# Optimization experiments

Measured on AMD Instinct MI355X. Metric: run time of the kernel, lower is better.

The kernel has to match this reference:

```python
import jax, jax.numpy as jnp
import numpy as np

MEAN, STD = 0.1307, 0.3081  # standard MNIST Normalization layer
FC = [784, 2048, 2048, 2048, 2048, 10]


def _forward_boxes(W, b, low, high):
    # swap bounds where weights are negative (interval arithmetic)
    Wn = jnp.where(W < 0, W, 0.0)
    Wp = jnp.where(W >= 0, W, 0.0)
    low_out = high @ Wn.T + low @ Wp.T + b
    high_out = low @ Wn.T + high @ Wp.T + b
    return low_out, high_out


def _abstract_relu(x, low, high):
    # vectorized DeepPoly relaxation (original loops per neuron)
    crossing = (low < 0) & (high > 0)
    denom = jnp.where(crossing, high - low, 1.0)  # safe denom
    ub_slope = jnp.where(crossing, high / denom, 0.0)
    ub_int = jnp.where(crossing, -(low * high) / denom, 0.0)
    lam = jnp.where(low * low > high * high, 0.0, 1.0)  # minimum-area lambda
    keep = jnp.where(high <= 0.0, 0.0, 1.0)  # identity diag unless dead neuron
    w_high = jnp.where(crossing, ub_slope, keep)
    w_low = jnp.where(crossing, lam, keep)
    b_high = ub_int
    x_out = jnp.maximum(x, 0.0)
    return x_out, w_low * low, w_high * high + b_high, (w_low, w_high, b_high)


def _back_sub_relu(M, w_high, w_low, b_high, is_high):
    # vectorized version of the original double python loop; w_* are the
    # relu diagonals ([in]), M is the accumulated backsub matrix [out,in]
    mask = (w_high != 0.0).astype(M.dtype)
    if is_high:
        out = jnp.where(M > 0, M * w_high, M * w_low) * mask
        bias = (jnp.maximum(M, 0.0) * mask) @ b_high
    else:
        out = jnp.where(M > 0, M * w_low, M * w_high) * mask
        bias = (jnp.minimum(M, 0.0) * mask) @ b_high
    return out, bias


def _back_sub(records, low0, high0, out_size):
    dt = low0.dtype
    Wl = jnp.eye(out_size, dtype=dt)
    Wh = jnp.eye(out_size, dtype=dt)
    bl = jnp.zeros(out_size, dtype=dt)
    bh = jnp.zeros(out_size, dtype=dt)
    for kind, data in reversed(records):
        if kind == 'linear':
            W, b = data
            bh = bh + Wh @ b
            bl = bl + Wl @ b
            Wh = Wh @ W
            Wl = Wl @ W
        else:  # relu
            wl, wh, bhr = data
            Wh, dbh = _back_sub_relu(Wh, wh, wl, bhr, True)
            Wl, dbl = _back_sub_relu(Wl, wh, wl, bhr, False)
            bh = bh + dbh
            bl = bl + dbl
    low_out, _ = _forward_boxes(Wl, bl, low0, high0)
    _, high_out = _forward_boxes(Wh, bh, low0, high0)
    return low_out, high_out


def _forward(x, low, high, params):
    norm = lambda t: ((t - MEAN) / STD).reshape(-1)
    x, low, high = norm(x), norm(low), norm(high)
    low0, high0 = low, high
    records = []
    n = len(params)
    for i, (W, b) in enumerate(params):
        x = W @ x + b
        records.append(('linear', (W, b)))
        # box bounds from forward_boxes are immediately replaced by backsub
        low, high = _back_sub(records, low0, high0, W.shape[0])
        if i + 1 < n:
            x, low, high, rdata = _abstract_relu(x, low, high)
            records.append(('relu', rdata))
    return x, low, high


def setup_inputs() -> dict:
    key = jax.random.key(0)
    ks = jax.random.split(key, 11)
    x = jax.random.normal(ks[0], (1, 1, 28, 28), dtype=jnp.float32)
    eps = 0.05
    inp = {"x": x, "low": x - eps, "high": x + eps}
    for i in range(5):
        fi, fo = FC[i], FC[i + 1]
        inp[f"W{i+1}"] = jax.random.normal(ks[1 + 2 * i], (fo, fi), dtype=jnp.float32) * float(1.0 / np.sqrt(fi))
        inp[f"b{i+1}"] = jax.random.normal(ks[2 + 2 * i], (fo,), dtype=jnp.float32) * 0.01
    return inp


def reference(x, low, high, W1, b1, W2, b2, W3, b3, W4, b4, W5, b5):
    params = [(W1, b1), (W2, b2), (W3, b3), (W4, b4), (W5, b5)]
    return _forward(x, low, high, params)
```

## Files before the change

### kernel.cpp

```cpp
#include <hip/hip_runtime.h>
#include <hip/hip_bf16.h>


#define MEAN_C 0.1307f
#define STD_C  0.3081f

#define OFF_X0     0u
#define OFF_X1     2048u
#define OFF_L0     4096u
#define OFF_H0     5120u
#define OFF_WL     6144u
#define OFF_WH     14336u
#define OFF_BHR    22528u
#define OFF_BOX    30720u
#define OFF_BIAS   34816u
#define OFF_B20    38912u
#define OFF_PPA    38944u
#define OFF_PPB    366624u
#define OFF_PPC    694304u
#define OFF_PPD    1021984u
#define OFF_WTH    1349664u
#define OFF_WTL    3446816u
#define OFF_AH0    5543968u
#define OFF_AL0    9738272u
#define OFF_AH1    13932576u
#define OFF_AL1    18126880u

typedef _Float16 half8 __attribute__((ext_vector_type(8)));
typedef float floatx4 __attribute__((ext_vector_type(4)));

__device__ __forceinline__ void gl2lds16(const void* g, void* l) {
    __builtin_amdgcn_global_load_lds(
        (const __attribute__((address_space(1))) unsigned int*)g,
        (__attribute__((address_space(3))) unsigned int*)l, 16, 0, 0);
}

__device__ __forceinline__ float blockReduce256(float v) {
    #pragma unroll
    for (int o = 32; o > 0; o >>= 1) v += __shfl_down(v, o, 64);
    __shared__ float sred[4];
    int w = threadIdx.x >> 6;
    if ((threadIdx.x & 63) == 0) sred[w] = v;
    __syncthreads();
    float r = 0.f;
    if (threadIdx.x == 0) r = sred[0] + sred[1] + sred[2] + sred[3];
    return r;
}

__device__ __forceinline__ float2 blockReduce256x2(float a, float b) {
    #pragma unroll
    for (int o = 32; o > 0; o >>= 1) {
        a += __shfl_down(a, o, 64);
        b += __shfl_down(b, o, 64);
    }
    __shared__ float sa[4], sb[4];
    int w = threadIdx.x >> 6;
    if ((threadIdx.x & 63) == 0) { sa[w] = a; sb[w] = b; }
    __syncthreads();
    float2 r = {0.f, 0.f};
    if (threadIdx.x == 0) {
        r.x = sa[0] + sa[1] + sa[2] + sa[3];
        r.y = sb[0] + sb[1] + sb[2] + sb[3];
    }
    return r;
}

__global__ void k_norm(const float* __restrict__ x, const float* __restrict__ lo,
                       const float* __restrict__ hi, float* __restrict__ ws) {
    int i = blockIdx.x * blockDim.x + threadIdx.x;
    if (i < 784) {
        ws[OFF_X0 + i] = (x[i]  - MEAN_C) / STD_C;
        ws[OFF_L0 + i] = (lo[i] - MEAN_C) / STD_C;
        ws[OFF_H0 + i] = (hi[i] - MEAN_C) / STD_C;
    } else if (i < 896) {
        ws[OFF_L0 + i] = 0.f;
        ws[OFF_H0 + i] = 0.f;
    }
}

__global__ void k_matvec(const float* __restrict__ W, const float* __restrict__ x,
                         const float* __restrict__ b, float* __restrict__ y, int k) {
    int r = blockIdx.x;
    const float* Wr = W + (size_t)r * k;
    float acc = 0.f;
    for (int c = threadIdx.x; c < k; c += 256) acc += Wr[c] * x[c];
    acc = blockReduce256(acc);
    if (threadIdx.x == 0) y[r] = acc + b[r];
}

__global__ void k_fboxes0(const float* __restrict__ W0, const float* __restrict__ b0,
                          const float* __restrict__ x0,
                          const float* __restrict__ lo0, const float* __restrict__ hi0,
                          float* __restrict__ box, float* __restrict__ xout) {
    int r = blockIdx.x;
    int srow = r & 2047;
    int is_high = r < 2048;
    const float* Wr = W0 + (size_t)srow * 784;
    float acc = 0.f, accx = 0.f;
    for (int c = threadIdx.x; c < 784; c += 256) {
        float m = Wr[c];
        if (is_high) acc += (m < 0.f) ? m * lo0[c] : m * hi0[c];
        else         acc += (m < 0.f) ? m * hi0[c] : m * lo0[c];
        accx += m * x0[c];
    }
    float2 rr = blockReduce256x2(acc, accx);
    if (threadIdx.x == 0) {
        box[r] = rr.x + b0[srow];
        if (is_high) xout[r] = rr.y + b0[r];
    }
}

__global__ __launch_bounds__(256) void k_relu_split(
        const float* __restrict__ Wi, const float* __restrict__ xin,
        const float* __restrict__ wl, const float* __restrict__ wh,
        const float* __restrict__ bhr, const float* __restrict__ bj,
        const float* __restrict__ bvi, float* __restrict__ bias,
        float* __restrict__ xout,
        _Float16* __restrict__ Ahi, _Float16* __restrict__ Alo) {
    int row = blockIdx.x;
    int is_high = row < 2048;
    int srow = row & 2047;
    const float* src = Wi + (size_t)srow * 2048;
    int c0 = threadIdx.x * 8;
    float mv[8], awl[8], awh[8], ab[8], abj[8], ax[8];
    *(float4*)&mv[0]  = *(const float4*)(src + c0);
    *(float4*)&mv[4]  = *(const float4*)(src + c0 + 4);
    *(float4*)&awl[0] = *(const float4*)(wl + c0);
    *(float4*)&awl[4] = *(const float4*)(wl + c0 + 4);
    *(float4*)&awh[0] = *(const float4*)(wh + c0);
    *(float4*)&awh[4] = *(const float4*)(wh + c0 + 4);
    *(float4*)&ab[0]  = *(const float4*)(bhr + c0);
    *(float4*)&ab[4]  = *(const float4*)(bhr + c0 + 4);
    *(float4*)&abj[0] = *(const float4*)(bj + c0);
    *(float4*)&abj[4] = *(const float4*)(bj + c0 + 4);
    *(float4*)&ax[0]  = *(const float4*)(xin + c0);
    *(float4*)&ax[4]  = *(const float4*)(xin + c0 + 4);
    float acc = 0.f, accx = 0.f;
    half8 hi, lo;
    #pragma unroll
    for (int e = 0; e < 8; e++) {
        float m = mv[e];
        float t, bt;
        if (is_high) { t = (m > 0.f) ? m * awh[e] : m * awl[e]; bt = fmaxf(m, 0.f) * ab[e]; }
        else         { t = (m > 0.f) ? m * awl[e] : m * awh[e]; bt = fminf(m, 0.f) * ab[e]; }
        acc += bt + t * abj[e];
        accx += m * ax[e];
        _Float16 h = (_Float16)t;
        hi[e] = h;
        lo[e] = (_Float16)(t - (float)h);
    }
    *(half8*)(Ahi + (size_t)row * 2048 + c0) = hi;
    *(half8*)(Alo + (size_t)row * 2048 + c0) = lo;
    float2 rr = blockReduce256x2(acc, accx);
    if (threadIdx.x == 0) {
        bias[row] = bvi[srow] + rr.x;
        if (is_high) xout[row] = rr.y + bvi[row];
    }
}

__global__ void k_transpose_split(const float* __restrict__ W, int NC,
                                  _Float16* __restrict__ Thi,
                                  _Float16* __restrict__ Tlo) {
    __shared__ float s[32][33];
    int c = threadIdx.x & 31;
    int r = threadIdx.x >> 5;
    #pragma unroll
    for (int rr = 0; rr < 4; rr++) {
        int k = blockIdx.y * 32 + r + rr * 8;
        int n = blockIdx.x * 32 + c;
        float v = (n < NC) ? W[(size_t)k * NC + n] : 0.f;
        s[c][r + rr * 8] = v;
    }
    __syncthreads();
    #pragma unroll
    for (int rr = 0; rr < 4; rr++) {
        int nl = r + rr * 8;
        float v = s[nl][c];
        _Float16 h = (_Float16)v;
        size_t o = (size_t)(blockIdx.x * 32 + nl) * 2048 + blockIdx.y * 32 + c;
        Thi[o] = h;
        Tlo[o] = (_Float16)(v - (float)h);
    }
}

template<int NT, int EPI>
__global__ __launch_bounds__(256, 2) void k_gemm(
        const _Float16* __restrict__ Ah, const _Float16* __restrict__ Al,
        const _Float16* __restrict__ Bh, const _Float16* __restrict__ Bl,
        const float* __restrict__ wl, const float* __restrict__ wh,
        const float* __restrict__ bhr, const float* __restrict__ bj,
        float* __restrict__ bias,
        _Float16* __restrict__ oAh, _Float16* __restrict__ oAl,
        const float* __restrict__ lo0, const float* __restrict__ hi0,
        float* __restrict__ box) {
    __shared__ _Float16 sA[2][2][4096];
    __shared__ _Float16 sB[2][2][NT * 1024];
    int tid = threadIdx.x;
    int row0 = blockIdx.y * 128, col0 = blockIdx.x * (NT * 32);

    int cr = tid >> 2;
    int q  = (tid & 3) ^ (cr & 3);
    const _Float16* gAh0 = Ah + (size_t)(row0 + cr) * 2048 + q * 8;
    const _Float16* gAh1 = gAh0 + (size_t)64 * 2048;
    const _Float16* gAl0 = Al + (size_t)(row0 + cr) * 2048 + q * 8;
    const _Float16* gAl1 = gAl0 + (size_t)64 * 2048;
    const _Float16* gBh0 = Bh + (size_t)(col0 + cr) * 2048 + q * 8;
    const _Float16* gBl0 = Bl + (size_t)(col0 + cr) * 2048 + q * 8;
    const _Float16* gBh1 = gBh0 + (size_t)64 * 2048;
    const _Float16* gBl1 = gBl0 + (size_t)64 * 2048;

    auto stage = [&](int k0, int b) {
        gl2lds16(gAh0 + k0, &sA[b][0][tid * 8]);
        gl2lds16(gAh1 + k0, &sA[b][0][tid * 8 + 2048]);
        gl2lds16(gAl0 + k0, &sA[b][1][tid * 8]);
        gl2lds16(gAl1 + k0, &sA[b][1][tid * 8 + 2048]);
        gl2lds16(gBh0 + k0, &sB[b][0][tid * 8]);
        gl2lds16(gBl0 + k0, &sB[b][1][tid * 8]);
        if (NT == 4) {
            gl2lds16(gBh1 + k0, &sB[b][0][tid * 8 + 2048]);
            gl2lds16(gBl1 + k0, &sB[b][1][tid * 8 + 2048]);
        }
    };

    int lane = tid & 63, wv = tid >> 6;
    int wm = wv & 1, wn = wv >> 1;
    int l15 = lane & 15, lq = lane >> 4;
    int soff = (lq ^ (l15 & 3)) * 8;
    int arow = wm * 64 + l15;
    int brow = wn * (NT * 16) + l15;

    floatx4 acc[4][NT];
    floatx4 z = {0.f, 0.f, 0.f, 0.f};
    #pragma unroll
    for (int i = 0; i < 4; i++)
        #pragma unroll
        for (int j = 0; j < NT; j++) acc[i][j] = z;

    stage(0, 0);
    for (int k0 = 0; k0 < 2048; k0 += 32) {
        int buf = (k0 >> 5) & 1;
        __syncthreads();
        if (k0 + 32 < 2048) stage(k0 + 32, buf ^ 1);
        half8 bh[NT], bl[NT];
        #pragma unroll
        for (int nt = 0; nt < NT; nt++) {
            bh[nt] = *(const half8*)&sB[buf][0][(brow + nt * 16) * 32 + soff];
            bl[nt] = *(const half8*)&sB[buf][1][(brow + nt * 16) * 32 + soff];
        }
        #pragma unroll
        for (int mt = 0; mt < 4; mt++) {
            half8 ah = *(const half8*)&sA[buf][0][(arow + mt * 16) * 32 + soff];
            half8 al = *(const half8*)&sA[buf][1][(arow + mt * 16) * 32 + soff];
            #pragma unroll
            for (int nt = 0; nt < NT; nt++) {
                acc[mt][nt] = __builtin_amdgcn_mfma_f32_16x16x32_f16(ah, bh[nt], acc[mt][nt], 0, 0, 0);
                acc[mt][nt] = __builtin_amdgcn_mfma_f32_16x16x32_f16(al, bh[nt], acc[mt][nt], 0, 0, 0);
                acc[mt][nt] = __builtin_amdgcn_mfma_f32_16x16x32_f16(ah, bl[nt], acc[mt][nt], 0, 0, 0);
            }
        }
    }

    int is_high = row0 < 2048;
    float bsum[4][4];
    #pragma unroll
    for (int mt = 0; mt < 4; mt++)
        #pragma unroll
        for (int r = 0; r < 4; r++) bsum[mt][r] = 0.f;

    #pragma unroll
    for (int nt = 0; nt < NT; nt++) {
        int gc = col0 + wn * (NT * 16) + nt * 16 + l15;
        if (EPI == 0) {
            float cwl = wl[gc], cwh = wh[gc], cbh = bhr[gc], cbj = bj[gc];
            #pragma unroll
            for (int mt = 0; mt < 4; mt++) {
                #pragma unroll
                for (int r = 0; r < 4; r++) {
                    float m = acc[mt][nt][r];
                    float t, bt;
                    if (is_high) { t = (m > 0.f) ? m * cwh : m * cwl; bt = fmaxf(m, 0.f) * cbh; }
                    else         { t = (m > 0.f) ? m * cwl : m * cwh; bt = fminf(m, 0.f) * cbh; }
                    bsum[mt][r] += bt + t * cbj;
                    int grow = row0 + wm * 64 + mt * 16 + lq * 4 + r;
                    size_t o = (size_t)grow * 2048 + gc;
                    _Float16 h = (_Float16)t;
                    oAh[o] = h;
                    oAl[o] = (_Float16)(t - (float)h);
                }
            }
        } else {
            float clo = lo0[gc], chi = hi0[gc];
            #pragma unroll
            for (int mt = 0; mt < 4; mt++) {
                #pragma unroll
                for (int r = 0; r < 4; r++) {
                    float m = acc[mt][nt][r];
                    float contrib;
                    if (is_high) contrib = (m < 0.f) ? m * clo : m * chi;
                    else         contrib = (m < 0.f) ? m * chi : m * clo;
                    bsum[mt][r] += contrib;
                }
            }
        }
    }
    #pragma unroll
    for (int mt = 0; mt < 4; mt++) {
        #pragma unroll
        for (int r = 0; r < 4; r++) {
            float v = bsum[mt][r];
            v += __shfl_xor(v, 1);
            v += __shfl_xor(v, 2);
            v += __shfl_xor(v, 4);
            v += __shfl_xor(v, 8);
            if (l15 == 0) {
                int grow = row0 + wm * 64 + mt * 16 + lq * 4 + r;
                if (EPI == 0) atomicAdd(&bias[grow], v);
                else          atomicAdd(&box[grow], v);
            }
        }
    }
}

__global__ __launch_bounds__(256) void k_skinny2(
        const float* __restrict__ src, int bcast,
        const float* __restrict__ wl, const float* __restrict__ wh,
        const float* __restrict__ W, int N, float* __restrict__ Ppart) {
    __shared__ float sA[20 * 256];
    __shared__ float sRed[20 * 128];
    int ky = blockIdx.y, k0 = ky * 256;
    int tid = threadIdx.x;
    for (int idx = tid; idx < 20 * 256; idx += 256) {
        int r = idx >> 8, c = idx & 255;
        int gc = k0 + c;
        float m;
        if (bcast) m = src[(size_t)(r % 10) * 2048 + gc];
        else {
            m = 0.f;
            #pragma unroll
            for (int p = 0; p < 8; p++)
                m += src[(size_t)p * 40960 + (size_t)r * 2048 + gc];
        }
        float t = (r < 10) ? ((m > 0.f) ? m * wh[gc] : m * wl[gc])
                           : ((m > 0.f) ? m * wl[gc] : m * wh[gc]);
        sA[idx] = t;
    }
    __syncthreads();
    int c = blockIdx.x * 128 + (tid & 127);
    int kh = tid >> 7;
    float acc[20];
    #pragma unroll
    for (int r = 0; r < 20; r++) acc[r] = 0.f;
    if (c < N) {
        const float* Wp = W + (size_t)(k0 + kh * 128) * N + c;
        for (int kk = 0; kk < 128; kk++) {
            float w = Wp[(size_t)kk * N];
            #pragma unroll
            for (int r = 0; r < 20; r++) acc[r] += sA[r * 256 + kh * 128 + kk] * w;
        }
    }
    if (kh == 1 && c < N) {
        #pragma unroll
        for (int r = 0; r < 20; r++) sRed[r * 128 + (tid & 127)] = acc[r];
    }
    __syncthreads();
    if (kh == 0 && c < N) {
        #pragma unroll
        for (int r = 0; r < 20; r++)
            Ppart[(size_t)ky * 40960 + (size_t)r * 2048 + c] =
                acc[r] + sRed[r * 128 + (tid & 127)];
    }
}

__global__ void k_bias20(const float* __restrict__ W4,
                         const float* __restrict__ PPa, const float* __restrict__ PPb,
                         const float* __restrict__ PPc,
                         const float* __restrict__ WLr, const float* __restrict__ WHr,
                         const float* __restrict__ BHr,
                         const float* __restrict__ b0, const float* __restrict__ b1,
                         const float* __restrict__ b2, const float* __restrict__ b3,
                         const float* __restrict__ b4,
                         float* __restrict__ bias20) {
    int row = blockIdx.x;
    int is_high = row < 10;
    int srow = row % 10;
    float acc = 0.f;
    for (int c = threadIdx.x; c < 2048; c += 256) {
        {
            float m = W4[(size_t)srow * 2048 + c];
            float wlv = WLr[3 * 2048 + c], whv = WHr[3 * 2048 + c], bhv = BHr[3 * 2048 + c];
            float t  = is_high ? ((m > 0.f) ? m * whv : m * wlv) : ((m > 0.f) ? m * wlv : m * whv);
            float bt = is_high ? fmaxf(m, 0.f) * bhv : fminf(m, 0.f) * bhv;
            acc += bt + t * b3[c];
        }
        {
            float m = 0.f;
            #pragma unroll
            for (int p = 0; p < 8; p++) m += PPa[(size_t)p * 40960 + (size_t)row * 2048 + c];
            float wlv = WLr[2 * 2048 + c], whv = WHr[2 * 2048 + c], bhv = BHr[2 * 2048 + c];
            float t  = is_high ? ((m > 0.f) ? m * whv : m * wlv) : ((m > 0.f) ? m * wlv : m * whv);
            float bt = is_high ? fmaxf(m, 0.f) * bhv : fminf(m, 0.f) * bhv;
            acc += bt + t * b2[c];
        }
        {
            float m = 0.f;
            #pragma unroll
            for (int p = 0; p < 8; p++) m += PPb[(size_t)p * 40960 + (size_t)row * 2048 + c];
            float wlv = WLr[1 * 2048 + c], whv = WHr[1 * 2048 + c], bhv = BHr[1 * 2048 + c];
            float t  = is_high ? ((m > 0.f) ? m * whv : m * wlv) : ((m > 0.f) ? m * wlv : m * whv);
            float bt = is_high ? fmaxf(m, 0.f) * bhv : fminf(m, 0.f) * bhv;
            acc += bt + t * b1[c];
        }
        {
            float m = 0.f;
            #pragma unroll
            for (int p = 0; p < 8; p++) m += PPc[(size_t)p * 40960 + (size_t)row * 2048 + c];
            float wlv = WLr[c], whv = WHr[c], bhv = BHr[c];
            float t  = is_high ? ((m > 0.f) ? m * whv : m * wlv) : ((m > 0.f) ? m * wlv : m * whv);
            float bt = is_high ? fmaxf(m, 0.f) * bhv : fminf(m, 0.f) * bhv;
            acc += bt + t * b0[c];
        }
    }
    acc = blockReduce256(acc);
    if (threadIdx.x == 0) bias20[row] = b4[srow] + acc;
}

__global__ void k_fbox20(const float* __restrict__ Ppart,
                         const float* __restrict__ bias20,
                         const float* __restrict__ lo0, const float* __restrict__ hi0,
                         float* __restrict__ out) {
    int row = blockIdx.x;
    int is_high = row < 10;
    float acc = 0.f;
    for (int c = threadIdx.x; c < 784; c += 256) {
        float m = 0.f;
        #pragma unroll
        for (int p = 0; p < 8; p++)
            m += Ppart[(size_t)p * 40960 + (size_t)row * 2048 + c];
        if (is_high) acc += (m < 0.f) ? m * lo0[c] : m * hi0[c];
        else         acc += (m < 0.f) ? m * hi0[c] : m * lo0[c];
    }
    acc = blockReduce256(acc);
    if (threadIdx.x == 0) {
        float v = acc + bias20[row];
        out[is_high ? (20 + row) : row] = v;
    }
}

__global__ void k_relu_rec(float* __restrict__ x, const float* __restrict__ box,
                           const float* __restrict__ bias,
                           float* __restrict__ wl, float* __restrict__ wh,
                           float* __restrict__ bhr) {
    int i = blockIdx.x * blockDim.x + threadIdx.x;
    float h = box[i]        + (bias ? bias[i]        : 0.f);
    float l = box[2048 + i] + (bias ? bias[2048 + i] : 0.f);
    float vwl, vwh, vbh;
    if (h <= 0.f)      { vwl = 0.f; vwh = 0.f; vbh = 0.f; }
    else if (l >= 0.f) { vwl = 1.f; vwh = 1.f; vbh = 0.f; }
    else {
        float d = h - l;
        vwh = h / d;
        vbh = -(l * h) / d;
        vwl = (l * l > h * h) ? 0.f : 1.f;
    }
    wl[i] = vwl; wh[i] = vwh; bhr[i] = vbh;
    x[i] = fmaxf(x[i], 0.f);
}

extern "C" void kernel_launch(void* const* d_in, const int* in_sizes, int n_in,
                              void* d_out, int out_size, void* d_ws, size_t ws_size,
                              hipStream_t stream) {
    const float* x_in  = (const float*)d_in[0];
    const float* lo_in = (const float*)d_in[1];
    const float* hi_in = (const float*)d_in[2];
    const float* W[5];
    const float* bv[5];
    for (int i = 0; i < 5; i++) {
        W[i]  = (const float*)d_in[3 + 2 * i];
        bv[i] = (const float*)d_in[4 + 2 * i];
    }
    float* ws = (float*)d_ws;
    float* out = (float*)d_out;

    float* X[2]   = {ws + OFF_X0, ws + OFF_X1};
    float* lo0    = ws + OFF_L0;
    float* hi0    = ws + OFF_H0;
    float* box    = ws + OFF_BOX;
    float* bias   = ws + OFF_BIAS;
    float* b20    = ws + OFF_B20;
    float* PPa    = ws + OFF_PPA;
    float* PPb    = ws + OFF_PPB;
    float* PPc    = ws + OFF_PPC;
    float* PPd    = ws + OFF_PPD;
    _Float16* WTh = (_Float16*)(ws + OFF_WTH);
    _Float16* WTl = (_Float16*)(ws + OFF_WTL);
    _Float16* AH[2] = {(_Float16*)(ws + OFF_AH0), (_Float16*)(ws + OFF_AH1)};
    _Float16* AL[2] = {(_Float16*)(ws + OFF_AL0), (_Float16*)(ws + OFF_AL1)};
    float* WLr = ws + OFF_WL;
    float* WHr = ws + OFF_WH;
    float* BHr = ws + OFF_BHR;

    k_norm<<<4, 256, 0, stream>>>(x_in, lo_in, hi_in, ws);

    k_fboxes0<<<4096, 256, 0, stream>>>(W[0], bv[0], X[0], lo0, hi0, box, X[1]);
    k_relu_rec<<<8, 256, 0, stream>>>(X[1], box, nullptr, WLr, WHr, BHr);

    int cur = 1;
    for (int i = 1; i <= 3; i++) {
        int nxt = cur ^ 1;
        k_relu_split<<<4096, 256, 0, stream>>>(
            W[i], X[cur],
            WLr + (i - 1) * 2048, WHr + (i - 1) * 2048,
            BHr + (i - 1) * 2048, bv[i - 1], bv[i], bias, X[nxt], AH[0], AL[0]);
        hipMemsetAsync(box, 0, 4096 * sizeof(float), stream);
        int p = 0;
        for (int j = i - 1; j >= 1; j--) {
            k_transpose_split<<<dim3(64, 64), 256, 0, stream>>>(W[j], 2048, WTh, WTl);
            k_gemm<4, 0><<<dim3(16, 32), 256, 0, stream>>>(
                AH[p], AL[p], WTh, WTl,
                WLr + (j - 1) * 2048, WHr + (j - 1) * 2048,
                BHr + (j - 1) * 2048, bv[j - 1], bias,
                AH[p ^ 1], AL[p ^ 1], nullptr, nullptr, nullptr);
            p ^= 1;
        }
        k_transpose_split<<<dim3(28, 64), 256, 0, stream>>>(W[0], 784, WTh, WTl);
        k_gemm<2, 1><<<dim3(14, 32), 256, 0, stream>>>(
            AH[p], AL[p], WTh, WTl,
            nullptr, nullptr, nullptr, nullptr, nullptr,
            nullptr, nullptr, lo0, hi0, box);
        k_relu_rec<<<8, 256, 0, stream>>>(X[nxt], box, bias,
                                          WLr + i * 2048, WHr + i * 2048,
                                          BHr + i * 2048);
        cur = nxt;
    }

    k_matvec<<<10, 256, 0, stream>>>(W[4], X[cur], bv[4], out, 2048);
    k_skinny2<<<dim3(16, 8), 256, 0, stream>>>(W[4], 1,
        WLr + 3 * 2048, WHr + 3 * 2048, W[3], 2048, PPa);
    k_skinny2<<<dim3(16, 8), 256, 0, stream>>>(PPa, 0,
        WLr + 2 * 2048, WHr + 2 * 2048, W[2], 2048, PPb);
    k_skinny2<<<dim3(16, 8), 256, 0, stream>>>(PPb, 0,
        WLr + 1 * 2048, WHr + 1 * 2048, W[1], 2048, PPc);
    k_skinny2<<<dim3(7, 8), 256, 0, stream>>>(PPc, 0,
        WLr, WHr, W[0], 784, PPd);
    k_bias20<<<20, 256, 0, stream>>>(W[4], PPa, PPb, PPc,
        WLr, WHr, BHr, bv[0], bv[1], bv[2], bv[3], bv[4], b20);
    k_fbox20<<<20, 256, 0, stream>>>(PPd, b20, lo0, hi0, out);
}
```

Before: 929.2 us.

## Transpose weights once, fuse relu records into split kernel, drop GEMM double-buffer

The fp16 hi/lo transposes of W0..W2 are computed once up front instead of inside every backsub iteration. The relu-relaxation computation and the box memset are folded into k_relu_split, and the final matvec into k_bias20, which removes several small launches. The GEMM drops LDS double buffering for a single buffer with two barriers per k-step. That halves shared memory, which may raise occupancy, but load latency is no longer overlapped with compute.

```diff
diff --git a/kernel.cpp b/kernel.cpp
--- a/kernel.cpp
+++ b/kernel.cpp
@@ -12,19 +12,25 @@
 #define OFF_WL     6144u
 #define OFF_WH     14336u
 #define OFF_BHR    22528u
-#define OFF_BOX    30720u
-#define OFF_BIAS   34816u
-#define OFF_B20    38912u
-#define OFF_PPA    38944u
-#define OFF_PPB    366624u
-#define OFF_PPC    694304u
-#define OFF_PPD    1021984u
-#define OFF_WTH    1349664u
-#define OFF_WTL    3446816u
-#define OFF_AH0    5543968u
-#define OFF_AL0    9738272u
-#define OFF_AH1    13932576u
-#define OFF_AL1    18126880u
+#define OFF_BOXA   30720u
+#define OFF_BOXB   34816u
+#define OFF_BIASA  38912u
+#define OFF_BIASB  43008u
+#define OFF_B20    47104u
+#define OFF_W0TH   47136u
+#define OFF_W0TL   964640u
+#define OFF_W1TH   1882144u
+#define OFF_W1TL   3979296u
+#define OFF_W2TH   6076448u
+#define OFF_W2TL   8173600u
+#define OFF_AH0    10270752u
+#define OFF_AL0    14465056u
+#define OFF_AH1    18659360u
+#define OFF_AL1    22853664u
+#define OFF_PPA    18659360u
+#define OFF_PPB    18987040u
+#define OFF_PPC    19314720u
+#define OFF_PPD    19642400u
 
 typedef _Float16 half8 __attribute__((ext_vector_type(8)));
 typedef float floatx4 __attribute__((ext_vector_type(4)));
@@ -63,6 +69,18 @@
         r.y = sb[0] + sb[1] + sb[2] + sb[3];
     }
     return r;
+}
+
+__device__ __forceinline__ void relu_rec_calc(float h, float l,
+                                              float& vwl, float& vwh, float& vbh) {
+    if (h <= 0.f)      { vwl = 0.f; vwh = 0.f; vbh = 0.f; }
+    else if (l >= 0.f) { vwl = 1.f; vwh = 1.f; vbh = 0.f; }
+    else {
+        float d = h - l;
+        vwh = h / d;
+        vbh = -(l * h) / d;
+        vwl = (l * l > h * h) ? 0.f : 1.f;
+    }
 }
 
 __global__ void k_norm(const float* __restrict__ x, const float* __restrict__ lo,
@@ -76,16 +94,6 @@
         ws[OFF_L0 + i] = 0.f;
         ws[OFF_H0 + i] = 0.f;
     }
-}
-
-__global__ void k_matvec(const float* __restrict__ W, const float* __restrict__ x,
-                         const float* __restrict__ b, float* __restrict__ y, int k) {
-    int r = blockIdx.x;
-    const float* Wr = W + (size_t)r * k;
-    float acc = 0.f;
-    for (int c = threadIdx.x; c < k; c += 256) acc += Wr[c] * x[c];
-    acc = blockReduce256(acc);
-    if (threadIdx.x == 0) y[r] = acc + b[r];
 }
 
 __global__ void k_fboxes0(const float* __restrict__ W0, const float* __restrict__ b0,
@@ -112,9 +120,10 @@
 
 __global__ __launch_bounds__(256) void k_relu_split(
         const float* __restrict__ Wi, const float* __restrict__ xin,
-        const float* __restrict__ wl, const float* __restrict__ wh,
-        const float* __restrict__ bhr, const float* __restrict__ bj,
-        const float* __restrict__ bvi, float* __restrict__ bias,
+        const float* __restrict__ boxPrev, const float* __restrict__ biasPrev,
+        float* __restrict__ recWL, float* __restrict__ recWH, float* __restrict__ recBH,
+        const float* __restrict__ bj, const float* __restrict__ bvi,
+        float* __restrict__ bias, float* __restrict__ boxOut,
         float* __restrict__ xout,
         _Float16* __restrict__ Ahi, _Float16* __restrict__ Alo) {
     int row = blockIdx.x;
@@ -122,38 +131,56 @@
     int srow = row & 2047;
     const float* src = Wi + (size_t)srow * 2048;
     int c0 = threadIdx.x * 8;
-    float mv[8], awl[8], awh[8], ab[8], abj[8], ax[8];
+    float mv[8], bxh[8], bxl[8], abj[8], ax[8];
     *(float4*)&mv[0]  = *(const float4*)(src + c0);
     *(float4*)&mv[4]  = *(const float4*)(src + c0 + 4);
-    *(float4*)&awl[0] = *(const float4*)(wl + c0);
-    *(float4*)&awl[4] = *(const float4*)(wl + c0 + 4);
-    *(float4*)&awh[0] = *(const float4*)(wh + c0);
-    *(float4*)&awh[4] = *(const float4*)(wh + c0 + 4);
-    *(float4*)&ab[0]  = *(const float4*)(bhr + c0);
-    *(float4*)&ab[4]  = *(const float4*)(bhr + c0 + 4);
+    *(float4*)&bxh[0] = *(const float4*)(boxPrev + c0);
+    *(float4*)&bxh[4] = *(const float4*)(boxPrev + c0 + 4);
+    *(float4*)&bxl[0] = *(const float4*)(boxPrev + 2048 + c0);
+    *(float4*)&bxl[4] = *(const float4*)(boxPrev + 2048 + c0 + 4);
     *(float4*)&abj[0] = *(const float4*)(bj + c0);
     *(float4*)&abj[4] = *(const float4*)(bj + c0 + 4);
     *(float4*)&ax[0]  = *(const float4*)(xin + c0);
     *(float4*)&ax[4]  = *(const float4*)(xin + c0 + 4);
+    if (biasPrev) {
+        float ph[8], pl[8];
+        *(float4*)&ph[0] = *(const float4*)(biasPrev + c0);
+        *(float4*)&ph[4] = *(const float4*)(biasPrev + c0 + 4);
+        *(float4*)&pl[0] = *(const float4*)(biasPrev + 2048 + c0);
+        *(float4*)&pl[4] = *(const float4*)(biasPrev + 2048 + c0 + 4);
+        #pragma unroll
+        for (int e = 0; e < 8; e++) { bxh[e] += ph[e]; bxl[e] += pl[e]; }
+    }
     float acc = 0.f, accx = 0.f;
+    float rl[8], rh[8], rb[8];
     half8 hi, lo;
     #pragma unroll
     for (int e = 0; e < 8; e++) {
+        relu_rec_calc(bxh[e], bxl[e], rl[e], rh[e], rb[e]);
         float m = mv[e];
         float t, bt;
-        if (is_high) { t = (m > 0.f) ? m * awh[e] : m * awl[e]; bt = fmaxf(m, 0.f) * ab[e]; }
-        else         { t = (m > 0.f) ? m * awl[e] : m * awh[e]; bt = fminf(m, 0.f) * ab[e]; }
+        if (is_high) { t = (m > 0.f) ? m * rh[e] : m * rl[e]; bt = fmaxf(m, 0.f) * rb[e]; }
+        else         { t = (m > 0.f) ? m * rl[e] : m * rh[e]; bt = fminf(m, 0.f) * rb[e]; }
         acc += bt + t * abj[e];
-        accx += m * ax[e];
+        accx += m * fmaxf(ax[e], 0.f);
         _Float16 h = (_Float16)t;
         hi[e] = h;
         lo[e] = (_Float16)(t - (float)h);
     }
     *(half8*)(Ahi + (size_t)row * 2048 + c0) = hi;
     *(half8*)(Alo + (size_t)row * 2048 + c0) = lo;
+    if (row == 0) {
+        *(float4*)(recWL + c0) = *(float4*)&rl[0];
+        *(float4*)(recWL + c0 + 4) = *(float4*)&rl[4];
+        *(float4*)(recWH + c0) = *(float4*)&rh[0];
+        *(float4*)(recWH + c0 + 4) = *(float4*)&rh[4];
+        *(float4*)(recBH + c0) = *(float4*)&rb[0];
+        *(float4*)(recBH + c0 + 4) = *(float4*)&rb[4];
+    }
     float2 rr = blockReduce256x2(acc, accx);
     if (threadIdx.x == 0) {
         bias[row] = bvi[srow] + rr.x;
+        boxOut[row] = 0.f;
         if (is_high) xout[row] = rr.y + bvi[row];
     }
 }
@@ -193,8 +220,8 @@
         _Float16* __restrict__ oAh, _Float16* __restrict__ oAl,
         const float* __restrict__ lo0, const float* __restrict__ hi0,
         float* __restrict__ box) {
-    __shared__ _Float16 sA[2][2][4096];
-    __shared__ _Float16 sB[2][2][NT * 1024];
+    __shared__ _Float16 sAh[128 * 32], sAl[128 * 32];
+    __shared__ _Float16 sBh[NT * 32 * 32], sBl[NT * 32 * 32];
     int tid = threadIdx.x;
     int row0 = blockIdx.y * 128, col0 = blockIdx.x * (NT * 32);
 
@@ -208,19 +235,14 @@
     const _Float16* gBl0 = Bl + (size_t)(col0 + cr) * 2048 + q * 8;
     const _Float16* gBh1 = gBh0 + (size_t)64 * 2048;
     const _Float16* gBl1 = gBl0 + (size_t)64 * 2048;
-
-    auto stage = [&](int k0, int b) {
-        gl2lds16(gAh0 + k0, &sA[b][0][tid * 8]);
-        gl2lds16(gAh1 + k0, &sA[b][0][tid * 8 + 2048]);
-        gl2lds16(gAl0 + k0, &sA[b][1][tid * 8]);
-        gl2lds16(gAl1 + k0, &sA[b][1][tid * 8 + 2048]);
-        gl2lds16(gBh0 + k0, &sB[b][0][tid * 8]);
-        gl2lds16(gBl0 + k0, &sB[b][1][tid * 8]);
-        if (NT == 4) {
-            gl2lds16(gBh1 + k0, &sB[b][0][tid * 8 + 2048]);
-            gl2lds16(gBl1 + k0, &sB[b][1][tid * 8 + 2048]);
-        }
-    };
+    _Float16* lAh0 = &sAh[tid * 8];
+    _Float16* lAh1 = &sAh[tid * 8 + 2048];
+    _Float16* lAl0 = &sAl[tid * 8];
+    _Float16* lAl1 = &sAl[tid * 8 + 2048];
+    _Float16* lBh0 = &sBh[tid * 8];
+    _Float16* lBl0 = &sBl[tid * 8];
+    _Float16* lBh1 = &sBh[tid * 8 + 2048];
+    _Float16* lBl1 = &sBl[tid * 8 + 2048];
 
     int lane = tid & 63, wv = tid >> 6;
     int wm = wv & 1, wn = wv >> 1;
@@ -236,21 +258,28 @@
         #pragma unroll
         for (int j = 0; j < NT; j++) acc[i][j] = z;
 
-    stage(0, 0);
     for (int k0 = 0; k0 < 2048; k0 += 32) {
-        int buf = (k0 >> 5) & 1;
+        gl2lds16(gAh0 + k0, lAh0);
+        gl2lds16(gAh1 + k0, lAh1);
+        gl2lds16(gAl0 + k0, lAl0);
+        gl2lds16(gAl1 + k0, lAl1);
+        gl2lds16(gBh0 + k0, lBh0);
+        gl2lds16(gBl0 + k0, lBl0);
+        if (NT == 4) {
+            gl2lds16(gBh1 + k0, lBh1);
+            gl2lds16(gBl1 + k0, lBl1);
+        }
         __syncthreads();
-        if (k0 + 32 < 2048) stage(k0 + 32, buf ^ 1);
         half8 bh[NT], bl[NT];
         #pragma unroll
         for (int nt = 0; nt < NT; nt++) {
-            bh[nt] = *(const half8*)&sB[buf][0][(brow + nt * 16) * 32 + soff];
-            bl[nt] = *(const half8*)&sB[buf][1][(brow + nt * 16) * 32 + soff];
+            bh[nt] = *(const half8*)&sBh[(brow + nt * 16) * 32 + soff];
+            bl[nt] = *(const half8*)&sBl[(brow + nt * 16) * 32 + soff];
         }
         #pragma unroll
         for (int mt = 0; mt < 4; mt++) {
-            half8 ah = *(const half8*)&sA[buf][0][(arow + mt * 16) * 32 + soff];
-            half8 al = *(const half8*)&sA[buf][1][(arow + mt * 16) * 32 + soff];
+            half8 ah = *(const half8*)&sAh[(arow + mt * 16) * 32 + soff];
+            half8 al = *(const half8*)&sAl[(arow + mt * 16) * 32 + soff];
             #pragma unroll
             for (int nt = 0; nt < NT; nt++) {
                 acc[mt][nt] = __builtin_amdgcn_mfma_f32_16x16x32_f16(ah, bh[nt], acc[mt][nt], 0, 0, 0);
@@ -258,6 +287,7 @@
                 acc[mt][nt] = __builtin_amdgcn_mfma_f32_16x16x32_f16(ah, bl[nt], acc[mt][nt], 0, 0, 0);
             }
         }
+        __syncthreads();
     }
 
     int is_high = row0 < 2048;
@@ -321,6 +351,17 @@
     }
 }
 
+__global__ void k_relu_rec(const float* __restrict__ box, const float* __restrict__ bias,
+                           float* __restrict__ wl, float* __restrict__ wh,
+                           float* __restrict__ bhr) {
+    int i = blockIdx.x * blockDim.x + threadIdx.x;
+    float h = box[i] + bias[i];
+    float l = box[2048 + i] + bias[2048 + i];
+    float vwl, vwh, vbh;
+    relu_rec_calc(h, l, vwl, vwh, vbh);
+    wl[i] = vwl; wh[i] = vwh; bhr[i] = vbh;
+}
+
 __global__ __launch_bounds__(256) void k_skinny2(
         const float* __restrict__ src, int bcast,
         const float* __restrict__ wl, const float* __restrict__ wh,
@@ -379,11 +420,12 @@
                          const float* __restrict__ b0, const float* __restrict__ b1,
                          const float* __restrict__ b2, const float* __restrict__ b3,
                          const float* __restrict__ b4,
-                         float* __restrict__ bias20) {
+                         const float* __restrict__ x3,
+                         float* __restrict__ bias20, float* __restrict__ out) {
     int row = blockIdx.x;
     int is_high = row < 10;
     int srow = row % 10;
-    float acc = 0.f;
+    float acc = 0.f, accx = 0.f;
     for (int c = threadIdx.x; c < 2048; c += 256) {
         {
             float m = W4[(size_t)srow * 2048 + c];
@@ -391,6 +433,7 @@
             float t  = is_high ? ((m > 0.f) ? m * whv : m * wlv) : ((m > 0.f) ? m * wlv : m * whv);
             float bt = is_high ? fmaxf(m, 0.f) * bhv : fminf(m, 0.f) * bhv;
             acc += bt + t * b3[c];
+            accx += m * fmaxf(x3[c], 0.f);
         }
         {
             float m = 0.f;
@@ -420,8 +463,11 @@
             acc += bt + t * b0[c];
         }
     }
-    acc = blockReduce256(acc);
-    if (threadIdx.x == 0) bias20[row] = b4[srow] + acc;
+    float2 rr = blockReduce256x2(acc, accx);
+    if (threadIdx.x == 0) {
+        bias20[row] = b4[srow] + rr.x;
+        if (is_high) out[row] = b4[row] + rr.y;
+    }
 }
 
 __global__ void k_fbox20(const float* __restrict__ Ppart,
@@ -444,26 +490,6 @@
         float v = acc + bias20[row];
         out[is_high ? (20 + row) : row] = v;
     }
-}
-
-__global__ void k_relu_rec(float* __restrict__ x, const float* __restrict__ box,
-                           const float* __restrict__ bias,
-                           float* __restrict__ wl, float* __restrict__ wh,
-                           float* __restrict__ bhr) {
-    int i = blockIdx.x * blockDim.x + threadIdx.x;
-    float h = box[i]        + (bias ? bias[i]        : 0.f);
-    float l = box[2048 + i] + (bias ? bias[2048 + i] : 0.f);
-    float vwl, vwh, vbh;
-    if (h <= 0.f)      { vwl = 0.f; vwh = 0.f; vbh = 0.f; }
-    else if (l >= 0.f) { vwl = 1.f; vwh = 1.f; vbh = 0.f; }
-    else {
-        float d = h - l;
-        vwh = h / d;
-        vbh = -(l * h) / d;
-        vwl = (l * l > h * h) ? 0.f : 1.f;
-    }
-    wl[i] = vwl; wh[i] = vwh; bhr[i] = vbh;
-    x[i] = fmaxf(x[i], 0.f);
 }
 
 extern "C" void kernel_launch(void* const* d_in, const int* in_sizes, int n_in,
@@ -481,18 +507,20 @@
     float* ws = (float*)d_ws;
     float* out = (float*)d_out;
 
-    float* X[2]   = {ws + OFF_X0, ws + OFF_X1};
-    float* lo0    = ws + OFF_L0;
-    float* hi0    = ws + OFF_H0;
-    float* box    = ws + OFF_BOX;
-    float* bias   = ws + OFF_BIAS;
-    float* b20    = ws + OFF_B20;
-    float* PPa    = ws + OFF_PPA;
-    float* PPb    = ws + OFF_PPB;
-    float* PPc    = ws + OFF_PPC;
-    float* PPd    = ws + OFF_PPD;
-    _Float16* WTh = (_Float16*)(ws + OFF_WTH);
-    _Float16* WTl = (_Float16*)(ws + OFF_WTL);
+    float* X[2]    = {ws + OFF_X0, ws + OFF_X1};
+    float* lo0     = ws + OFF_L0;
+    float* hi0     = ws + OFF_H0;
+    float* BOX[2]  = {ws + OFF_BOXA, ws + OFF_BOXB};
+    float* BIAS[2] = {ws + OFF_BIASA, ws + OFF_BIASB};
+    float* b20     = ws + OFF_B20;
+    float* PPa     = ws + OFF_PPA;
+    float* PPb     = ws + OFF_PPB;
+    float* PPc     = ws + OFF_PPC;
+    float* PPd     = ws + OFF_PPD;
+    _Float16* WT_H[3] = {(_Float16*)(ws + OFF_W0TH), (_Float16*)(ws + OFF_W1TH),
+                         (_Float16*)(ws + OFF_W2TH)};
+    _Float16* WT_L[3] = {(_Float16*)(ws + OFF_W0TL), (_Float16*)(ws + OFF_W1TL),
+                         (_Float16*)(ws + OFF_W2TL)};
     _Float16* AH[2] = {(_Float16*)(ws + OFF_AH0), (_Float16*)(ws + OFF_AH1)};
     _Float16* AL[2] = {(_Float16*)(ws + OFF_AL0), (_Float16*)(ws + OFF_AL1)};
     float* WLr = ws + OFF_WL;
@@ -500,40 +528,42 @@
     float* BHr = ws + OFF_BHR;
 
     k_norm<<<4, 256, 0, stream>>>(x_in, lo_in, hi_in, ws);
-
-    k_fboxes0<<<4096, 256, 0, stream>>>(W[0], bv[0], X[0], lo0, hi0, box, X[1]);
-    k_relu_rec<<<8, 256, 0, stream>>>(X[1], box, nullptr, WLr, WHr, BHr);
-
-    int cur = 1;
+    k_transpose_split<<<dim3(28, 64), 256, 0, stream>>>(W[0], 784, WT_H[0], WT_L[0]);
+    k_transpose_split<<<dim3(64, 64), 256, 0, stream>>>(W[1], 2048, WT_H[1], WT_L[1]);
+    k_transpose_split<<<dim3(64, 64), 256, 0, stream>>>(W[2], 2048, WT_H[2], WT_L[2]);
+
+    k_fboxes0<<<4096, 256, 0, stream>>>(W[0], bv[0], X[0], lo0, hi0, BOX[0], X[1]);
+
+    int xcur = 1, bprev = 0;
+    const float* biasPrev = nullptr;
     for (int i = 1; i <= 3; i++) {
-        int nxt = cur ^ 1;
+        int xnxt = xcur ^ 1;
+        int bcur = bprev ^ 1;
+        float* biasCur = BIAS[(i - 1) & 1];
         k_relu_split<<<4096, 256, 0, stream>>>(
-            W[i], X[cur],
-            WLr + (i - 1) * 2048, WHr + (i - 1) * 2048,
-            BHr + (i - 1) * 2048, bv[i - 1], bv[i], bias, X[nxt], AH[0], AL[0]);
-        hipMemsetAsync(box, 0, 4096 * sizeof(float), stream);
+            W[i], X[xcur], BOX[bprev], biasPrev,
+            WLr + (i - 1) * 2048, WHr + (i - 1) * 2048, BHr + (i - 1) * 2048,
+            bv[i - 1], bv[i], biasCur, BOX[bcur], X[xnxt], AH[0], AL[0]);
         int p = 0;
         for (int j = i - 1; j >= 1; j--) {
-            k_transpose_split<<<dim3(64, 64), 256, 0, stream>>>(W[j], 2048, WTh, WTl);
             k_gemm<4, 0><<<dim3(16, 32), 256, 0, stream>>>(
-                AH[p], AL[p], WTh, WTl,
+                AH[p], AL[p], WT_H[j], WT_L[j],
                 WLr + (j - 1) * 2048, WHr + (j - 1) * 2048,
-                BHr + (j - 1) * 2048, bv[j - 1], bias,
+                BHr + (j - 1) * 2048, bv[j - 1], biasCur,
                 AH[p ^ 1], AL[p ^ 1], nullptr, nullptr, nullptr);
             p ^= 1;
         }
-        k_transpose_split<<<dim3(28, 64), 256, 0, stream>>>(W[0], 784, WTh, WTl);
         k_gemm<2, 1><<<dim3(14, 32), 256, 0, stream>>>(
-            AH[p], AL[p], WTh, WTl,
+            AH[p], AL[p], WT_H[0], WT_L[0],
             nullptr, nullptr, nullptr, nullptr, nullptr,
-            nullptr, nullptr, lo0, hi0, box);
-        k_relu_rec<<<8, 256, 0, stream>>>(X[nxt], box, bias,
-                                          WLr + i * 2048, WHr + i * 2048,
-                                          BHr + i * 2048);
-        cur = nxt;
-    }
-
-    k_matvec<<<10, 256, 0, stream>>>(W[4], X[cur], bv[4], out, 2048);
+            nullptr, nullptr, lo0, hi0, BOX[bcur]);
+        biasPrev = biasCur;
+        bprev = bcur;
+        xcur = xnxt;
+    }
+    k_relu_rec<<<8, 256, 0, stream>>>(BOX[bprev], BIAS[0],
+                                      WLr + 3 * 2048, WHr + 3 * 2048, BHr + 3 * 2048);
+
     k_skinny2<<<dim3(16, 8), 256, 0, stream>>>(W[4], 1,
         WLr + 3 * 2048, WHr + 3 * 2048, W[3], 2048, PPa);
     k_skinny2<<<dim3(16, 8), 256, 0, stream>>>(PPa, 0,
@@ -543,6 +573,6 @@
     k_skinny2<<<dim3(7, 8), 256, 0, stream>>>(PPc, 0,
         WLr, WHr, W[0], 784, PPd);
     k_bias20<<<20, 256, 0, stream>>>(W[4], PPa, PPb, PPc,
-        WLr, WHr, BHr, bv[0], bv[1], bv[2], bv[3], bv[4], b20);
+        WLr, WHr, BHr, bv[0], bv[1], bv[2], bv[3], bv[4], X[xcur], b20, out);
     k_fbox20<<<20, 256, 0, stream>>>(PPd, b20, lo0, hi0, out);
 }
```

Result: faster. 906.8 us (-2.4%).
